# Kernel optimization log

Measured on AMD Instinct MI355X. Metric: run time of the kernel, lower is better.

## Reference

```python
import jax, jax.numpy as jnp
import numpy as np

B, S, H = 256, 1, 2048
Q_SIZE = 4096        # num_heads * head_dim = 32 * 128
QKV = 4 * H          # expected_linear_qkv = 8192
K_SZ = 4             # conv kernel size
C = 32               # ssm channels
WSCALE = 0.02


def setup_inputs() -> dict:
    key = jax.random.key(0)
    ks = jax.random.split(key, 13)
    return {
        "hidden_states": jax.random.normal(ks[0], (B, S, H), jnp.float32),
        "W_qkv": jax.random.normal(ks[1], (QKV, H), jnp.float32) * WSCALE,
        "b_qkv": jax.random.normal(ks[2], (QKV,), jnp.float32) * WSCALE,
        "W_gate": jax.random.normal(ks[3], (2 * H, H), jnp.float32) * WSCALE,
        "W_alpha": jax.random.normal(ks[4], (C, H), jnp.float32) * WSCALE,
        "W_beta": jax.random.normal(ks[5], (C, H), jnp.float32) * WSCALE,
        "W_out": jax.random.normal(ks[6], (H, 2 * H), jnp.float32) * WSCALE,
        "ssm_state_a": jax.random.normal(ks[7], (C,), jnp.float32),
        "ssm_dt_bias": jax.random.normal(ks[8], (C,), jnp.float32),
        "ssm_norm_weight": jnp.ones((128,), jnp.float32),
        "conv_kernel": jax.random.normal(ks[9], (QKV, K_SZ), jnp.float32) * WSCALE,
        "ssm_state": jax.random.normal(ks[10], (B, C), jnp.float32),
        "conv_state": jax.random.normal(ks[11], (B, K_SZ, QKV), jnp.float32),
    }


def reference(hidden_states, W_qkv, b_qkv, W_gate, W_alpha, W_beta, W_out,
              ssm_state_a, ssm_dt_bias, ssm_norm_weight, conv_kernel,
              ssm_state, conv_state):
    bsz = hidden_states.shape[0]
    # qkv projection (decode: only last token matters downstream)
    qkv = jnp.einsum('bsh,dh->bsd', hidden_states, W_qkv) + b_qkv  # [B,S,4H]
    mixed_qkv = qkv[:, -1, :].astype(jnp.float32)                  # [B,4H]
    hidden_last = hidden_states[:, -1, :]                          # [B,H]

    # roll conv state and append current token, then causal conv1d step
    cs = jnp.concatenate([conv_state[:, 1:, :], mixed_qkv[:, None, :]], axis=1)  # [B,K,4H]
    conv_out = jnp.einsum('bkd,dk->bd', cs, conv_kernel)           # [B,4H]

    target_size = conv_out.shape[-1] - Q_SIZE                      # 2H = 4096
    k_size = target_size // 2                                      # 2048
    core_base = conv_out[:, Q_SIZE:]                               # [B,2H]
    k_proj = core_base[:, :k_size]
    v_proj = core_base[:, k_size:]

    # alpha/beta gating of the SSM state
    a = hidden_last @ W_alpha.T                                    # [B,C]
    b = hidden_last @ W_beta.T                                     # [B,C]
    g = -jnp.exp(ssm_state_a)[None, :] * jax.nn.softplus(a + ssm_dt_bias[None, :])
    beta = jax.nn.sigmoid(b)

    group_width = k_size // C                                      # 64
    v_group = v_proj[:, :group_width * C].reshape(bsz, C, group_width).mean(-1)
    k_group = k_proj[:, :group_width * C].reshape(bsz, C, group_width).mean(-1)

    new_state = jnp.exp(g) * ssm_state + beta * v_group            # [B,C]
    state_signal = new_state * jax.nn.sigmoid(k_group)             # [B,C]

    repeat_factor = target_size // C                               # 128
    expanded = jnp.repeat(state_signal, repeat_factor, axis=-1)[:, :target_size]

    core = core_base + expanded
    core = core * jax.lax.rsqrt(jnp.mean(core * core, axis=-1, keepdims=True) + 1e-6)
    gate = jax.nn.sigmoid(hidden_last @ W_gate.T).astype(jnp.float32)
    core = core * gate * jnp.mean(ssm_norm_weight)
    core = core.astype(hidden_states.dtype)

    out = (core @ W_out.T)[:, None, :]                             # [B,1,H]
    return out
```

## Files before the change

### kernel.cpp

```cpp
#include <hip/hip_runtime.h>
#include <hip/hip_bf16.h>
#include <stdint.h>

#define BSZ 256
#define NQ 4096
#define N1 8320
#define K1 2048
#define N3 2048
#define K3 4096
#define Z3 4

typedef __attribute__((ext_vector_type(8))) short bf16x8;
typedef __attribute__((ext_vector_type(4))) float f32x4;

__device__ __forceinline__ unsigned short f2bf(float f) {
  union { float f; unsigned u; } v; v.f = f;
  unsigned r = v.u + 0x7fffu + ((v.u >> 16) & 1u);
  return (unsigned short)(r >> 16);
}

__device__ __forceinline__ bf16x8 pack8(float4 a, float4 b) {
  union { bf16x8 v; unsigned short u[8]; } o;
  o.u[0] = f2bf(a.x); o.u[1] = f2bf(a.y); o.u[2] = f2bf(a.z); o.u[3] = f2bf(a.w);
  o.u[4] = f2bf(b.x); o.u[5] = f2bf(b.y); o.u[6] = f2bf(b.z); o.u[7] = f2bf(b.w);
  return o.v;
}

__device__ __forceinline__ void gload_lds16(const void* g, void* lds_uniform) {
  __builtin_amdgcn_global_load_lds(
      (const __attribute__((address_space(1))) unsigned int*)g,
      (__attribute__((address_space(3))) unsigned int*)lds_uniform, 16, 0, 0);
}

__global__ __launch_bounds__(256) void cvt_kernel(const float* __restrict__ x,
                                                  unsigned short* __restrict__ y) {
  int i = (blockIdx.x * 256 + threadIdx.x) * 8;
  float4 a = *(const float4*)(x + i);
  float4 b = *(const float4*)(x + i + 4);
  ushort4 o0 = { f2bf(a.x), f2bf(a.y), f2bf(a.z), f2bf(a.w) };
  ushort4 o1 = { f2bf(b.x), f2bf(b.y), f2bf(b.z), f2bf(b.w) };
  *(ushort4*)(y + i) = o0;
  *(ushort4*)(y + i + 4) = o1;
}


__global__ __launch_bounds__(256, 3) void gemm1_kernel(
    const unsigned short* __restrict__ A16,
    const float* __restrict__ Wqkv, const float* __restrict__ Wgate,
    const float* __restrict__ Walpha, const float* __restrict__ Wbeta,
    float* __restrict__ P) {
  __shared__ __align__(16) unsigned short sA[2][128 * 64];
  __shared__ __align__(16) float sB[2][32 * 64];
  const int tid = threadIdx.x, lane = tid & 63, wv = tid >> 6;
  const int wr = wv >> 1, wc = wv & 1, l15 = lane & 15;
  const int rt = blockIdx.x * 128;
  const int n0 = blockIdx.y * 32;

  const char* aS[4]; char* aD[4];
#pragma unroll
  for (int t = 0; t < 4; t++) {
    int s = wv * 4 + t;
    int m = 8 * s + (lane >> 3);
    int c = (lane & 7) ^ ((lane >> 3) & 7);
    aS[t] = (const char*)(A16 + (size_t)(rt + m) * K1) + c * 16;
    aD[t] = (char*)(&sA[0][0]) + s * 1024;
  }
  const char* bS[2]; char* bD[2];
#pragma unroll
  for (int t = 0; t < 2; t++) {
    int s = wv * 2 + t;
    int n = 4 * s + (lane >> 4);
    int c = (lane & 15) ^ (n & 15);
    int ng = n0 + n;
    const float* base;
    if (ng < 4096)       base = Wqkv  + (size_t)(4096 + ng) * K1;
    else if (ng < 8192)  base = Wgate + (size_t)(ng - 4096) * K1;
    else if (ng < 8224)  base = Walpha + (size_t)(ng - 8192) * K1;
    else if (ng < 8256)  base = Wbeta + (size_t)(ng - 8224) * K1;
    else                 base = Walpha;
    bS[t] = (const char*)base + c * 16;
    bD[t] = (char*)(&sB[0][0]) + s * 1024;
  }

  f32x4 acc[4];
#pragma unroll
  for (int i = 0; i < 4; i++) { f32x4 z = {0.f, 0.f, 0.f, 0.f}; acc[i] = z; }

#pragma unroll
  for (int t = 0; t < 4; t++) gload_lds16(aS[t], aD[t]);
#pragma unroll
  for (int t = 0; t < 2; t++) gload_lds16(bS[t], bD[t]);
  __syncthreads();

  int cur = 0;
  for (int it = 0; it < 32; it++) {
    if (it < 31) {
#pragma unroll
      for (int t = 0; t < 4; t++)
        gload_lds16(aS[t] + (it + 1) * 128, aD[t] + (cur ^ 1) * 16384);
#pragma unroll
      for (int t = 0; t < 2; t++)
        gload_lds16(bS[t] + (it + 1) * 256, bD[t] + (cur ^ 1) * 8192);
    }
    __builtin_amdgcn_sched_barrier(0);
    const char* sAb = (const char*)sA + cur * 16384;
    const char* sBb = (const char*)sB + cur * 8192;
#pragma unroll
    for (int ks2 = 0; ks2 < 2; ks2++) {
      int nr = wc * 16 + l15;
      int c0 = ks2 * 8 + (lane >> 4) * 2;
      float4 b0 = *(const float4*)(sBb + nr * 256 + ((c0 ^ (nr & 15)) * 16));
      float4 b1 = *(const float4*)(sBb + nr * 256 + (((c0 + 1) ^ (nr & 15)) * 16));
      bf16x8 bF = pack8(b0, b1);
#pragma unroll
      for (int i = 0; i < 4; i++) {
        int m = wr * 64 + i * 16 + l15;
        int cA = ks2 * 4 + (lane >> 4);
        bf16x8 aF = *(const bf16x8*)(sAb + m * 128 + ((cA ^ (m & 7)) * 16));
        acc[i] = __builtin_amdgcn_mfma_f32_16x16x32_bf16(aF, bF, acc[i], 0, 0, 0);
      }
    }
    __syncthreads();
    cur ^= 1;
  }

#pragma unroll
  for (int i = 0; i < 4; i++) {
    int row = rt + wr * 64 + i * 16 + (lane >> 4) * 4;
    int col = n0 + wc * 16 + l15;
#pragma unroll
    for (int r = 0; r < 4; r++)
      P[(size_t)(row + r) * N1 + col] = acc[i][r];
  }
}

__global__ __launch_bounds__(512) void fuse_kernel(
    const float* __restrict__ P,
    const float* __restrict__ bqkv,
    const float* __restrict__ ck,
    const float* __restrict__ cstate,
    const float* __restrict__ ssa,
    const float* __restrict__ dtb,
    const float* __restrict__ nw,
    const float* __restrict__ sstate,
    unsigned short* __restrict__ C16) {
  __shared__ __align__(16) float cb[4096];
  __shared__ float gsum[64];
  __shared__ float ssl[32];
  __shared__ float red[16];
  const int b = blockIdx.x, tid = threadIdx.x;
  const int lane = tid & 63, wv = tid >> 6;
  const float* P0 = P + (size_t)b * N1;

  if (wv == 0) {
    float m = nw[lane] + nw[lane + 64];
#pragma unroll
    for (int off = 32; off; off >>= 1) m += __shfl_down(m, off, 64);
    if (lane == 0) red[8] = m * (1.f / 128.f);
  }

#pragma unroll
  for (int it = 0; it < 2; it++) {
    int j = (it * 512 + tid) * 4;
    float4 q0 = *(const float4*)(P0 + j);
    float4 bq = *(const float4*)(bqkv + NQ + j);
    float mqx = q0.x + bq.x, mqy = q0.y + bq.y;
    float mqz = q0.z + bq.z, mqw = q0.w + bq.w;
    const float* csb = cstate + (size_t)b * 4 * 8192 + NQ + j;
    float4 c1 = *(const float4*)(csb + 8192);
    float4 c2 = *(const float4*)(csb + 16384);
    float4 c3 = *(const float4*)(csb + 24576);
    float4 k0v = *(const float4*)(ck + (size_t)(NQ + j) * 4);
    float4 k1v = *(const float4*)(ck + (size_t)(NQ + j + 1) * 4);
    float4 k2v = *(const float4*)(ck + (size_t)(NQ + j + 2) * 4);
    float4 k3v = *(const float4*)(ck + (size_t)(NQ + j + 3) * 4);
    float4 cbv;
    cbv.x = c1.x * k0v.x + c2.x * k0v.y + c3.x * k0v.z + mqx * k0v.w;
    cbv.y = c1.y * k1v.x + c2.y * k1v.y + c3.y * k1v.z + mqy * k1v.w;
    cbv.z = c1.z * k2v.x + c2.z * k2v.y + c3.z * k2v.z + mqz * k2v.w;
    cbv.w = c1.w * k3v.x + c2.w * k3v.y + c3.w * k3v.z + mqw * k3v.w;
    *(float4*)(cb + j) = cbv;
    float s = cbv.x + cbv.y + cbv.z + cbv.w;
    s += __shfl_xor(s, 1, 64); s += __shfl_xor(s, 2, 64);
    s += __shfl_xor(s, 4, 64); s += __shfl_xor(s, 8, 64);
    if ((lane & 15) == 0) gsum[(it * 512 + tid) >> 4] = s;
  }
  __syncthreads();

  if (tid < 32) {
    float a  = P0[8192 + tid];
    float bc = P0[8224 + tid];
    float kg = gsum[tid] * (1.f / 64.f);
    float vg = gsum[32 + tid] * (1.f / 64.f);
    float x = a + dtb[tid];
    float sp = fmaxf(x, 0.f) + log1pf(expf(-fabsf(x)));
    float g = -expf(ssa[tid]) * sp;
    float beta = 1.f / (1.f + expf(-bc));
    float ns = expf(g) * sstate[b * 32 + tid] + beta * vg;
    ssl[tid] = ns / (1.f + expf(-kg));
  }
  __syncthreads();

  float sq = 0.f;
  float4 c1r[2];
#pragma unroll
  for (int it = 0; it < 2; it++) {
    int j = (it * 512 + tid) * 4;
    float4 v = *(const float4*)(cb + j);
    float sv = ssl[j >> 7];
    v.x += sv; v.y += sv; v.z += sv; v.w += sv;
    c1r[it] = v;
    sq += v.x * v.x + v.y * v.y + v.z * v.z + v.w * v.w;
  }
#pragma unroll
  for (int off = 32; off; off >>= 1) sq += __shfl_down(sq, off, 64);
  if (lane == 0) red[wv] = sq;
  __syncthreads();
  if (tid == 0) {
    float t = red[0] + red[1] + red[2] + red[3] + red[4] + red[5] + red[6] + red[7];
    red[9] = rsqrtf(t * (1.f / 4096.f) + 1e-6f);
  }
  __syncthreads();
  float rms = red[9], mwv = red[8];

#pragma unroll
  for (int it = 0; it < 2; it++) {
    int j = (it * 512 + tid) * 4;
    float4 g0x = *(const float4*)(P0 + NQ + j);
    float4 v = c1r[it];
    float ox = v.x * rms * mwv / (1.f + expf(-g0x.x));
    float oy = v.y * rms * mwv / (1.f + expf(-g0x.y));
    float oz = v.z * rms * mwv / (1.f + expf(-g0x.z));
    float ow = v.w * rms * mwv / (1.f + expf(-g0x.w));
    ushort4 u = { f2bf(ox), f2bf(oy), f2bf(oz), f2bf(ow) };
    *(ushort4*)(C16 + (size_t)b * 4096 + j) = u;
  }
}

__global__ __launch_bounds__(256, 3) void gemm3_kernel(
    const unsigned short* __restrict__ A16,
    const float* __restrict__ Wout,
    float* __restrict__ OP) {
  __shared__ __align__(16) unsigned short sA[2][128 * 64];
  __shared__ __align__(16) float sB[2][32 * 64];
  const int tid = threadIdx.x, lane = tid & 63, wv = tid >> 6;
  const int wr = wv >> 1, wc = wv & 1, l15 = lane & 15;
  const int rt = blockIdx.x * 128;
  const int n0 = blockIdx.y * 32;
  const int kb = blockIdx.z * 1024;

  const char* aS[4]; char* aD[4];
#pragma unroll
  for (int t = 0; t < 4; t++) {
    int s = wv * 4 + t;
    int m = 8 * s + (lane >> 3);
    int c = (lane & 7) ^ ((lane >> 3) & 7);
    aS[t] = (const char*)(A16 + (size_t)(rt + m) * K3 + kb) + c * 16;
    aD[t] = (char*)(&sA[0][0]) + s * 1024;
  }
  const char* bS[2]; char* bD[2];
#pragma unroll
  for (int t = 0; t < 2; t++) {
    int s = wv * 2 + t;
    int n = 4 * s + (lane >> 4);
    int c = (lane & 15) ^ (n & 15);
    bS[t] = (const char*)(Wout + (size_t)(n0 + n) * K3 + kb) + c * 16;
    bD[t] = (char*)(&sB[0][0]) + s * 1024;
  }

  f32x4 acc[4];
#pragma unroll
  for (int i = 0; i < 4; i++) { f32x4 z = {0.f, 0.f, 0.f, 0.f}; acc[i] = z; }

#pragma unroll
  for (int t = 0; t < 4; t++) gload_lds16(aS[t], aD[t]);
#pragma unroll
  for (int t = 0; t < 2; t++) gload_lds16(bS[t], bD[t]);
  __syncthreads();

  int cur = 0;
  for (int it = 0; it < 16; it++) {
    if (it < 15) {
#pragma unroll
      for (int t = 0; t < 4; t++)
        gload_lds16(aS[t] + (it + 1) * 128, aD[t] + (cur ^ 1) * 16384);
#pragma unroll
      for (int t = 0; t < 2; t++)
        gload_lds16(bS[t] + (it + 1) * 256, bD[t] + (cur ^ 1) * 8192);
    }
    __builtin_amdgcn_sched_barrier(0);
    const char* sAb = (const char*)sA + cur * 16384;
    const char* sBb = (const char*)sB + cur * 8192;
#pragma unroll
    for (int ks2 = 0; ks2 < 2; ks2++) {
      int nr = wc * 16 + l15;
      int c0 = ks2 * 8 + (lane >> 4) * 2;
      float4 b0 = *(const float4*)(sBb + nr * 256 + ((c0 ^ (nr & 15)) * 16));
      float4 b1 = *(const float4*)(sBb + nr * 256 + (((c0 + 1) ^ (nr & 15)) * 16));
      bf16x8 bF = pack8(b0, b1);
#pragma unroll
      for (int i = 0; i < 4; i++) {
        int m = wr * 64 + i * 16 + l15;
        int cA = ks2 * 4 + (lane >> 4);
        bf16x8 aF = *(const bf16x8*)(sAb + m * 128 + ((cA ^ (m & 7)) * 16));
        acc[i] = __builtin_amdgcn_mfma_f32_16x16x32_bf16(aF, bF, acc[i], 0, 0, 0);
      }
    }
    __syncthreads();
    cur ^= 1;
  }

  float* Oz = OP + (size_t)blockIdx.z * ((size_t)BSZ * N3);
#pragma unroll
  for (int i = 0; i < 4; i++) {
    int row = rt + wr * 64 + i * 16 + (lane >> 4) * 4;
    int col = n0 + wc * 16 + l15;
#pragma unroll
    for (int r = 0; r < 4; r++)
      Oz[(size_t)(row + r) * N3 + col] = acc[i][r];
  }
}

__global__ __launch_bounds__(256) void reduce_kernel(const float* __restrict__ OP,
                                                     float* __restrict__ out) {
  int i = (blockIdx.x * 256 + threadIdx.x) * 4;
  float4 s = *(const float4*)(OP + i);
#pragma unroll
  for (int z = 1; z < Z3; z++) {
    float4 v = *(const float4*)(OP + (size_t)z * BSZ * N3 + i);
    s.x += v.x; s.y += v.y; s.z += v.z; s.w += v.w;
  }
  *(float4*)(out + i) = s;
}

extern "C" void kernel_launch(void* const* d_in, const int* in_sizes, int n_in,
                              void* d_out, int out_size, void* d_ws, size_t ws_size,
                              hipStream_t stream) {
  const float* hidden = (const float*)d_in[0];
  const float* Wqkv   = (const float*)d_in[1];
  const float* bqkv   = (const float*)d_in[2];
  const float* Wgate  = (const float*)d_in[3];
  const float* Walpha = (const float*)d_in[4];
  const float* Wbeta  = (const float*)d_in[5];
  const float* Wout   = (const float*)d_in[6];
  const float* ssa    = (const float*)d_in[7];
  const float* dtb    = (const float*)d_in[8];
  const float* nw     = (const float*)d_in[9];
  const float* ck     = (const float*)d_in[10];
  const float* sstate = (const float*)d_in[11];
  const float* cstate = (const float*)d_in[12];
  float* out = (float*)d_out;

  char* ws = (char*)d_ws;
  unsigned short* A16 = (unsigned short*)ws;
  float* P   = (float*)(ws + (1 << 20));
  unsigned short* C16 = (unsigned short*)(ws + (1 << 20) + 8519680);
  float* OP  = (float*)(ws + (1 << 20) + 8519680 + (2 << 20));

  cvt_kernel<<<256, 256, 0, stream>>>(hidden, A16);
  gemm1_kernel<<<dim3(2, 260, 1), 256, 0, stream>>>(A16, Wqkv, Wgate, Walpha, Wbeta, P);
  fuse_kernel<<<256, 512, 0, stream>>>(P, bqkv, ck, cstate, ssa, dtb, nw, sstate, C16);
  gemm3_kernel<<<dim3(2, 64, Z3), 256, 0, stream>>>(C16, Wout, OP);
  reduce_kernel<<<512, 256, 0, stream>>>(OP, out);
}
```

Baseline: 232.5 us.

## Triple-buffer LDS tiles in both GEMMs with one barrier per iteration

Moves both bf16 MFMA GEMMs from a double-buffered LDS pipeline with two __syncthreads per k-step to a three-stage ring buffer. Each step waits only for the tile two loads back (vmcnt(6)) and then issues a single barrier. This keeps two tiles of global-to-LDS loads in flight and removes one barrier per iteration. The cost is 50% more LDS per block, so launch bounds drop from 3 to 2 blocks per CU, which lowers occupancy.

```diff
diff --git a/kernel.cpp b/kernel.cpp
--- a/kernel.cpp
+++ b/kernel.cpp
@@ -12,6 +12,9 @@
 
 typedef __attribute__((ext_vector_type(8))) short bf16x8;
 typedef __attribute__((ext_vector_type(4))) float f32x4;
+
+#define WAIT6_BARRIER() asm volatile("s_waitcnt vmcnt(6)\n\ts_barrier" ::: "memory")
+#define WAIT0_BARRIER() asm volatile("s_waitcnt vmcnt(0)\n\ts_barrier" ::: "memory")
 
 __device__ __forceinline__ unsigned short f2bf(float f) {
   union { float f; unsigned u; } v; v.f = f;
@@ -44,13 +47,13 @@
 }
 
 
-__global__ __launch_bounds__(256, 3) void gemm1_kernel(
+__global__ __launch_bounds__(256, 2) void gemm1_kernel(
     const unsigned short* __restrict__ A16,
     const float* __restrict__ Wqkv, const float* __restrict__ Wgate,
     const float* __restrict__ Walpha, const float* __restrict__ Wbeta,
     float* __restrict__ P) {
-  __shared__ __align__(16) unsigned short sA[2][128 * 64];
-  __shared__ __align__(16) float sB[2][32 * 64];
+  __shared__ __align__(16) unsigned short sA[3][128 * 64];
+  __shared__ __align__(16) float sB[3][32 * 64];
   const int tid = threadIdx.x, lane = tid & 63, wv = tid >> 6;
   const int wr = wv >> 1, wc = wv & 1, l15 = lane & 15;
   const int rt = blockIdx.x * 128;
@@ -90,21 +93,24 @@
   for (int t = 0; t < 4; t++) gload_lds16(aS[t], aD[t]);
 #pragma unroll
   for (int t = 0; t < 2; t++) gload_lds16(bS[t], bD[t]);
-  __syncthreads();
-
-  int cur = 0;
-  for (int it = 0; it < 32; it++) {
-    if (it < 31) {
+#pragma unroll
+  for (int t = 0; t < 4; t++) gload_lds16(aS[t] + 128, aD[t] + 16384);
+#pragma unroll
+  for (int t = 0; t < 2; t++) gload_lds16(bS[t] + 256, bD[t] + 8192);
+
+  int bc = 0, bi = 2;
+  for (int it = 0; it < 31; ++it) {
+    WAIT6_BARRIER();
+    if (it < 30) {
 #pragma unroll
       for (int t = 0; t < 4; t++)
-        gload_lds16(aS[t] + (it + 1) * 128, aD[t] + (cur ^ 1) * 16384);
+        gload_lds16(aS[t] + (it + 2) * 128, aD[t] + bi * 16384);
 #pragma unroll
       for (int t = 0; t < 2; t++)
-        gload_lds16(bS[t] + (it + 1) * 256, bD[t] + (cur ^ 1) * 8192);
-    }
-    __builtin_amdgcn_sched_barrier(0);
-    const char* sAb = (const char*)sA + cur * 16384;
-    const char* sBb = (const char*)sB + cur * 8192;
+        gload_lds16(bS[t] + (it + 2) * 256, bD[t] + bi * 8192);
+    }
+    const char* sAb = (const char*)sA + bc * 16384;
+    const char* sBb = (const char*)sB + bc * 8192;
 #pragma unroll
     for (int ks2 = 0; ks2 < 2; ks2++) {
       int nr = wc * 16 + l15;
@@ -120,8 +126,28 @@
         acc[i] = __builtin_amdgcn_mfma_f32_16x16x32_bf16(aF, bF, acc[i], 0, 0, 0);
       }
     }
-    __syncthreads();
-    cur ^= 1;
+    bc = (bc == 2) ? 0 : bc + 1;
+    bi = (bi == 2) ? 0 : bi + 1;
+  }
+  WAIT0_BARRIER();
+  {
+    const char* sAb = (const char*)sA + bc * 16384;
+    const char* sBb = (const char*)sB + bc * 8192;
+#pragma unroll
+    for (int ks2 = 0; ks2 < 2; ks2++) {
+      int nr = wc * 16 + l15;
+      int c0 = ks2 * 8 + (lane >> 4) * 2;
+      float4 b0 = *(const float4*)(sBb + nr * 256 + ((c0 ^ (nr & 15)) * 16));
+      float4 b1 = *(const float4*)(sBb + nr * 256 + (((c0 + 1) ^ (nr & 15)) * 16));
+      bf16x8 bF = pack8(b0, b1);
+#pragma unroll
+      for (int i = 0; i < 4; i++) {
+        int m = wr * 64 + i * 16 + l15;
+        int cA = ks2 * 4 + (lane >> 4);
+        bf16x8 aF = *(const bf16x8*)(sAb + m * 128 + ((cA ^ (m & 7)) * 16));
+        acc[i] = __builtin_amdgcn_mfma_f32_16x16x32_bf16(aF, bF, acc[i], 0, 0, 0);
+      }
+    }
   }
 
 #pragma unroll
@@ -237,12 +263,12 @@
   }
 }
 
-__global__ __launch_bounds__(256, 3) void gemm3_kernel(
+__global__ __launch_bounds__(256, 2) void gemm3_kernel(
     const unsigned short* __restrict__ A16,
     const float* __restrict__ Wout,
     float* __restrict__ OP) {
-  __shared__ __align__(16) unsigned short sA[2][128 * 64];
-  __shared__ __align__(16) float sB[2][32 * 64];
+  __shared__ __align__(16) unsigned short sA[3][128 * 64];
+  __shared__ __align__(16) float sB[3][32 * 64];
   const int tid = threadIdx.x, lane = tid & 63, wv = tid >> 6;
   const int wr = wv >> 1, wc = wv & 1, l15 = lane & 15;
   const int rt = blockIdx.x * 128;
@@ -276,21 +302,24 @@
   for (int t = 0; t < 4; t++) gload_lds16(aS[t], aD[t]);
 #pragma unroll
   for (int t = 0; t < 2; t++) gload_lds16(bS[t], bD[t]);
-  __syncthreads();
-
-  int cur = 0;
-  for (int it = 0; it < 16; it++) {
-    if (it < 15) {
+#pragma unroll
+  for (int t = 0; t < 4; t++) gload_lds16(aS[t] + 128, aD[t] + 16384);
+#pragma unroll
+  for (int t = 0; t < 2; t++) gload_lds16(bS[t] + 256, bD[t] + 8192);
+
+  int bc = 0, bi = 2;
+  for (int it = 0; it < 15; ++it) {
+    WAIT6_BARRIER();
+    if (it < 14) {
 #pragma unroll
       for (int t = 0; t < 4; t++)
-        gload_lds16(aS[t] + (it + 1) * 128, aD[t] + (cur ^ 1) * 16384);
+        gload_lds16(aS[t] + (it + 2) * 128, aD[t] + bi * 16384);
 #pragma unroll
       for (int t = 0; t < 2; t++)
-        gload_lds16(bS[t] + (it + 1) * 256, bD[t] + (cur ^ 1) * 8192);
-    }
-    __builtin_amdgcn_sched_barrier(0);
-    const char* sAb = (const char*)sA + cur * 16384;
-    const char* sBb = (const char*)sB + cur * 8192;
+        gload_lds16(bS[t] + (it + 2) * 256, bD[t] + bi * 8192);
+    }
+    const char* sAb = (const char*)sA + bc * 16384;
+    const char* sBb = (const char*)sB + bc * 8192;
 #pragma unroll
     for (int ks2 = 0; ks2 < 2; ks2++) {
       int nr = wc * 16 + l15;
@@ -306,8 +335,28 @@
         acc[i] = __builtin_amdgcn_mfma_f32_16x16x32_bf16(aF, bF, acc[i], 0, 0, 0);
       }
     }
-    __syncthreads();
-    cur ^= 1;
+    bc = (bc == 2) ? 0 : bc + 1;
+    bi = (bi == 2) ? 0 : bi + 1;
+  }
+  WAIT0_BARRIER();
+  {
+    const char* sAb = (const char*)sA + bc * 16384;
+    const char* sBb = (const char*)sB + bc * 8192;
+#pragma unroll
+    for (int ks2 = 0; ks2 < 2; ks2++) {
+      int nr = wc * 16 + l15;
+      int c0 = ks2 * 8 + (lane >> 4) * 2;
+      float4 b0 = *(const float4*)(sBb + nr * 256 + ((c0 ^ (nr & 15)) * 16));
+      float4 b1 = *(const float4*)(sBb + nr * 256 + (((c0 + 1) ^ (nr & 15)) * 16));
+      bf16x8 bF = pack8(b0, b1);
+#pragma unroll
+      for (int i = 0; i < 4; i++) {
+        int m = wr * 64 + i * 16 + l15;
+        int cA = ks2 * 4 + (lane >> 4);
+        bf16x8 aF = *(const bf16x8*)(sAb + m * 128 + ((cA ^ (m & 7)) * 16));
+        acc[i] = __builtin_amdgcn_mfma_f32_16x16x32_bf16(aF, bF, acc[i], 0, 0, 0);
+      }
+    }
   }
 
   float* Oz = OP + (size_t)blockIdx.z * ((size_t)BSZ * N3);
```

New measurement: 256.4 us. +10.3%, slower.

## Replace LDS-staged GEMM tiles with per-wave direct global-load MFMA strips

Applied to the files above, without the earlier changes.

Both GEMMs drop the double-buffered LDS staging with global_load_lds and barriers. Each wave now computes a 16x32 output strip, loading A and fp32 B fragments straight from global memory into registers. The bf16 packing also switches to the built-in paired float-to-bf16 conversion. This removes LDS traffic and syncs, but each weight row is re-read by every M strip (16 strips over 256 rows) instead of once per 128-row tile. That multiplies global and L2 traffic for the large fp32 weights.

```diff
diff --git a/kernel.cpp b/kernel.cpp
--- a/kernel.cpp
+++ b/kernel.cpp
@@ -20,16 +20,12 @@
 }
 
 __device__ __forceinline__ bf16x8 pack8(float4 a, float4 b) {
-  union { bf16x8 v; unsigned short u[8]; } o;
-  o.u[0] = f2bf(a.x); o.u[1] = f2bf(a.y); o.u[2] = f2bf(a.z); o.u[3] = f2bf(a.w);
-  o.u[4] = f2bf(b.x); o.u[5] = f2bf(b.y); o.u[6] = f2bf(b.z); o.u[7] = f2bf(b.w);
+  union { bf16x8 v; __hip_bfloat162 h[4]; } o;
+  o.h[0] = __float22bfloat162_rn(float2{a.x, a.y});
+  o.h[1] = __float22bfloat162_rn(float2{a.z, a.w});
+  o.h[2] = __float22bfloat162_rn(float2{b.x, b.y});
+  o.h[3] = __float22bfloat162_rn(float2{b.z, b.w});
   return o.v;
-}
-
-__device__ __forceinline__ void gload_lds16(const void* g, void* lds_uniform) {
-  __builtin_amdgcn_global_load_lds(
-      (const __attribute__((address_space(1))) unsigned int*)g,
-      (__attribute__((address_space(3))) unsigned int*)lds_uniform, 16, 0, 0);
 }
 
 __global__ __launch_bounds__(256) void cvt_kernel(const float* __restrict__ x,
@@ -44,93 +40,59 @@
 }
 
 
-__global__ __launch_bounds__(256, 3) void gemm1_kernel(
+__global__ __launch_bounds__(256) void gemm1_kernel(
     const unsigned short* __restrict__ A16,
     const float* __restrict__ Wqkv, const float* __restrict__ Wgate,
     const float* __restrict__ Walpha, const float* __restrict__ Wbeta,
     float* __restrict__ P) {
-  __shared__ __align__(16) unsigned short sA[2][128 * 64];
-  __shared__ __align__(16) float sB[2][32 * 64];
   const int tid = threadIdx.x, lane = tid & 63, wv = tid >> 6;
-  const int wr = wv >> 1, wc = wv & 1, l15 = lane & 15;
-  const int rt = blockIdx.x * 128;
-  const int n0 = blockIdx.y * 32;
-
-  const char* aS[4]; char* aD[4];
-#pragma unroll
-  for (int t = 0; t < 4; t++) {
-    int s = wv * 4 + t;
-    int m = 8 * s + (lane >> 3);
-    int c = (lane & 7) ^ ((lane >> 3) & 7);
-    aS[t] = (const char*)(A16 + (size_t)(rt + m) * K1) + c * 16;
-    aD[t] = (char*)(&sA[0][0]) + s * 1024;
-  }
-  const char* bS[2]; char* bD[2];
-#pragma unroll
-  for (int t = 0; t < 2; t++) {
-    int s = wv * 2 + t;
-    int n = 4 * s + (lane >> 4);
-    int c = (lane & 15) ^ (n & 15);
-    int ng = n0 + n;
-    const float* base;
-    if (ng < 4096)       base = Wqkv  + (size_t)(4096 + ng) * K1;
-    else if (ng < 8192)  base = Wgate + (size_t)(ng - 4096) * K1;
-    else if (ng < 8224)  base = Walpha + (size_t)(ng - 8192) * K1;
-    else if (ng < 8256)  base = Wbeta + (size_t)(ng - 8224) * K1;
-    else                 base = Walpha;
-    bS[t] = (const char*)base + c * 16;
-    bD[t] = (char*)(&sB[0][0]) + s * 1024;
-  }
-
-  f32x4 acc[4];
-#pragma unroll
-  for (int i = 0; i < 4; i++) { f32x4 z = {0.f, 0.f, 0.f, 0.f}; acc[i] = z; }
-
-#pragma unroll
-  for (int t = 0; t < 4; t++) gload_lds16(aS[t], aD[t]);
-#pragma unroll
-  for (int t = 0; t < 2; t++) gload_lds16(bS[t], bD[t]);
-  __syncthreads();
-
-  int cur = 0;
-  for (int it = 0; it < 32; it++) {
-    if (it < 31) {
-#pragma unroll
-      for (int t = 0; t < 4; t++)
-        gload_lds16(aS[t] + (it + 1) * 128, aD[t] + (cur ^ 1) * 16384);
-#pragma unroll
-      for (int t = 0; t < 2; t++)
-        gload_lds16(bS[t] + (it + 1) * 256, bD[t] + (cur ^ 1) * 8192);
-    }
-    __builtin_amdgcn_sched_barrier(0);
-    const char* sAb = (const char*)sA + cur * 16384;
-    const char* sBb = (const char*)sB + cur * 8192;
-#pragma unroll
-    for (int ks2 = 0; ks2 < 2; ks2++) {
-      int nr = wc * 16 + l15;
-      int c0 = ks2 * 8 + (lane >> 4) * 2;
-      float4 b0 = *(const float4*)(sBb + nr * 256 + ((c0 ^ (nr & 15)) * 16));
-      float4 b1 = *(const float4*)(sBb + nr * 256 + (((c0 + 1) ^ (nr & 15)) * 16));
-      bf16x8 bF = pack8(b0, b1);
-#pragma unroll
-      for (int i = 0; i < 4; i++) {
-        int m = wr * 64 + i * 16 + l15;
-        int cA = ks2 * 4 + (lane >> 4);
-        bf16x8 aF = *(const bf16x8*)(sAb + m * 128 + ((cA ^ (m & 7)) * 16));
-        acc[i] = __builtin_amdgcn_mfma_f32_16x16x32_bf16(aF, bF, acc[i], 0, 0, 0);
-      }
-    }
-    __syncthreads();
-    cur ^= 1;
-  }
-
-#pragma unroll
-  for (int i = 0; i < 4; i++) {
-    int row = rt + wr * 64 + i * 16 + (lane >> 4) * 4;
-    int col = n0 + wc * 16 + l15;
-#pragma unroll
-    for (int r = 0; r < 4; r++)
-      P[(size_t)(row + r) * N1 + col] = acc[i][r];
+  const int l15 = lane & 15, hi8 = (lane >> 4) * 8;
+  const int wid = blockIdx.x * 4 + wv;
+  const int nidx = wid % 260;
+  const int strip = wid / 260;
+  const int m0 = strip * 16;
+  const int n0 = nidx * 32;
+
+  const unsigned short* Arow = A16 + (size_t)(m0 + l15) * K1 + hi8;
+  const float* Brow0;
+  const float* Brow1;
+  {
+    int ng0 = n0 + l15;
+    int ng1 = n0 + 16 + l15;
+    const float* b0;
+    const float* b1;
+    if (ng0 < 4096)       b0 = Wqkv  + (size_t)(4096 + ng0) * K1;
+    else if (ng0 < 8192)  b0 = Wgate + (size_t)(ng0 - 4096) * K1;
+    else if (ng0 < 8224)  b0 = Walpha + (size_t)(ng0 - 8192) * K1;
+    else if (ng0 < 8256)  b0 = Wbeta + (size_t)(ng0 - 8224) * K1;
+    else                  b0 = Walpha + (size_t)l15 * K1;
+    if (ng1 < 4096)       b1 = Wqkv  + (size_t)(4096 + ng1) * K1;
+    else if (ng1 < 8192)  b1 = Wgate + (size_t)(ng1 - 4096) * K1;
+    else if (ng1 < 8224)  b1 = Walpha + (size_t)(ng1 - 8192) * K1;
+    else if (ng1 < 8256)  b1 = Wbeta + (size_t)(ng1 - 8224) * K1;
+    else                  b1 = Walpha + (size_t)l15 * K1;
+    Brow0 = b0 + hi8;
+    Brow1 = b1 + hi8;
+  }
+
+  f32x4 acc0 = {0.f, 0.f, 0.f, 0.f};
+  f32x4 acc1 = {0.f, 0.f, 0.f, 0.f};
+#pragma unroll 4
+  for (int kk = 0; kk < K1; kk += 32) {
+    bf16x8 aF = *(const bf16x8*)(Arow + kk);
+    float4 b0a = *(const float4*)(Brow0 + kk);
+    float4 b0b = *(const float4*)(Brow0 + kk + 4);
+    float4 b1a = *(const float4*)(Brow1 + kk);
+    float4 b1b = *(const float4*)(Brow1 + kk + 4);
+    acc0 = __builtin_amdgcn_mfma_f32_16x16x32_bf16(aF, pack8(b0a, b0b), acc0, 0, 0, 0);
+    acc1 = __builtin_amdgcn_mfma_f32_16x16x32_bf16(aF, pack8(b1a, b1b), acc1, 0, 0, 0);
+  }
+
+  const int row = m0 + (lane >> 4) * 4;
+#pragma unroll
+  for (int r = 0; r < 4; r++) {
+    P[(size_t)(row + r) * N1 + (n0 + l15)] = acc0[r];
+    P[(size_t)(row + r) * N1 + (n0 + 16 + l15)] = acc1[r];
   }
 }
 
@@ -237,87 +199,43 @@
   }
 }
 
-__global__ __launch_bounds__(256, 3) void gemm3_kernel(
+__global__ __launch_bounds__(256) void gemm3_kernel(
     const unsigned short* __restrict__ A16,
     const float* __restrict__ Wout,
     float* __restrict__ OP) {
-  __shared__ __align__(16) unsigned short sA[2][128 * 64];
-  __shared__ __align__(16) float sB[2][32 * 64];
   const int tid = threadIdx.x, lane = tid & 63, wv = tid >> 6;
-  const int wr = wv >> 1, wc = wv & 1, l15 = lane & 15;
-  const int rt = blockIdx.x * 128;
-  const int n0 = blockIdx.y * 32;
-  const int kb = blockIdx.z * 1024;
-
-  const char* aS[4]; char* aD[4];
-#pragma unroll
-  for (int t = 0; t < 4; t++) {
-    int s = wv * 4 + t;
-    int m = 8 * s + (lane >> 3);
-    int c = (lane & 7) ^ ((lane >> 3) & 7);
-    aS[t] = (const char*)(A16 + (size_t)(rt + m) * K3 + kb) + c * 16;
-    aD[t] = (char*)(&sA[0][0]) + s * 1024;
-  }
-  const char* bS[2]; char* bD[2];
-#pragma unroll
-  for (int t = 0; t < 2; t++) {
-    int s = wv * 2 + t;
-    int n = 4 * s + (lane >> 4);
-    int c = (lane & 15) ^ (n & 15);
-    bS[t] = (const char*)(Wout + (size_t)(n0 + n) * K3 + kb) + c * 16;
-    bD[t] = (char*)(&sB[0][0]) + s * 1024;
-  }
-
-  f32x4 acc[4];
-#pragma unroll
-  for (int i = 0; i < 4; i++) { f32x4 z = {0.f, 0.f, 0.f, 0.f}; acc[i] = z; }
-
-#pragma unroll
-  for (int t = 0; t < 4; t++) gload_lds16(aS[t], aD[t]);
-#pragma unroll
-  for (int t = 0; t < 2; t++) gload_lds16(bS[t], bD[t]);
-  __syncthreads();
-
-  int cur = 0;
-  for (int it = 0; it < 16; it++) {
-    if (it < 15) {
-#pragma unroll
-      for (int t = 0; t < 4; t++)
-        gload_lds16(aS[t] + (it + 1) * 128, aD[t] + (cur ^ 1) * 16384);
-#pragma unroll
-      for (int t = 0; t < 2; t++)
-        gload_lds16(bS[t] + (it + 1) * 256, bD[t] + (cur ^ 1) * 8192);
-    }
-    __builtin_amdgcn_sched_barrier(0);
-    const char* sAb = (const char*)sA + cur * 16384;
-    const char* sBb = (const char*)sB + cur * 8192;
-#pragma unroll
-    for (int ks2 = 0; ks2 < 2; ks2++) {
-      int nr = wc * 16 + l15;
-      int c0 = ks2 * 8 + (lane >> 4) * 2;
-      float4 b0 = *(const float4*)(sBb + nr * 256 + ((c0 ^ (nr & 15)) * 16));
-      float4 b1 = *(const float4*)(sBb + nr * 256 + (((c0 + 1) ^ (nr & 15)) * 16));
-      bf16x8 bF = pack8(b0, b1);
-#pragma unroll
-      for (int i = 0; i < 4; i++) {
-        int m = wr * 64 + i * 16 + l15;
-        int cA = ks2 * 4 + (lane >> 4);
-        bf16x8 aF = *(const bf16x8*)(sAb + m * 128 + ((cA ^ (m & 7)) * 16));
-        acc[i] = __builtin_amdgcn_mfma_f32_16x16x32_bf16(aF, bF, acc[i], 0, 0, 0);
-      }
-    }
-    __syncthreads();
-    cur ^= 1;
-  }
-
-  float* Oz = OP + (size_t)blockIdx.z * ((size_t)BSZ * N3);
-#pragma unroll
-  for (int i = 0; i < 4; i++) {
-    int row = rt + wr * 64 + i * 16 + (lane >> 4) * 4;
-    int col = n0 + wc * 16 + l15;
-#pragma unroll
-    for (int r = 0; r < 4; r++)
-      Oz[(size_t)(row + r) * N3 + col] = acc[i][r];
+  const int l15 = lane & 15, hi8 = (lane >> 4) * 8;
+  const int wid = blockIdx.x * 4 + wv;
+  const int z = blockIdx.y;
+  const int nidx = wid % 64;
+  const int strip = wid / 64;
+  const int m0 = strip * 16;
+  const int n0 = nidx * 32;
+  const int kb = z * 1024;
+
+  const unsigned short* Arow = A16 + (size_t)(m0 + l15) * K3 + kb + hi8;
+  const float* Brow0 = Wout + (size_t)(n0 + l15) * K3 + kb + hi8;
+  const float* Brow1 = Wout + (size_t)(n0 + 16 + l15) * K3 + kb + hi8;
+
+  f32x4 acc0 = {0.f, 0.f, 0.f, 0.f};
+  f32x4 acc1 = {0.f, 0.f, 0.f, 0.f};
+#pragma unroll 4
+  for (int kk = 0; kk < 1024; kk += 32) {
+    bf16x8 aF = *(const bf16x8*)(Arow + kk);
+    float4 b0a = *(const float4*)(Brow0 + kk);
+    float4 b0b = *(const float4*)(Brow0 + kk + 4);
+    float4 b1a = *(const float4*)(Brow1 + kk);
+    float4 b1b = *(const float4*)(Brow1 + kk + 4);
+    acc0 = __builtin_amdgcn_mfma_f32_16x16x32_bf16(aF, pack8(b0a, b0b), acc0, 0, 0, 0);
+    acc1 = __builtin_amdgcn_mfma_f32_16x16x32_bf16(aF, pack8(b1a, b1b), acc1, 0, 0, 0);
+  }
+
+  float* Oz = OP + (size_t)z * ((size_t)BSZ * N3);
+  const int row = m0 + (lane >> 4) * 4;
+#pragma unroll
+  for (int r = 0; r < 4; r++) {
+    Oz[(size_t)(row + r) * N3 + (n0 + l15)] = acc0[r];
+    Oz[(size_t)(row + r) * N3 + (n0 + 16 + l15)] = acc1[r];
   }
 }
 
@@ -358,8 +276,8 @@
   float* OP  = (float*)(ws + (1 << 20) + 8519680 + (2 << 20));
 
   cvt_kernel<<<256, 256, 0, stream>>>(hidden, A16);
-  gemm1_kernel<<<dim3(2, 260, 1), 256, 0, stream>>>(A16, Wqkv, Wgate, Walpha, Wbeta, P);
+  gemm1_kernel<<<1040, 256, 0, stream>>>(A16, Wqkv, Wgate, Walpha, Wbeta, P);
   fuse_kernel<<<256, 512, 0, stream>>>(P, bqkv, ck, cstate, ssa, dtb, nw, sstate, C16);
-  gemm3_kernel<<<dim3(2, 64, Z3), 256, 0, stream>>>(C16, Wout, OP);
+  gemm3_kernel<<<dim3(256, 4), 256, 0, stream>>>(C16, Wout, OP);
   reduce_kernel<<<512, 256, 0, stream>>>(OP, out);
 }
```

After: 418.8 us. 80.1% more time.
